# Performance work log

Hardware: AMD Instinct MI355X
Metric: run time of the kernel (lower is better)

The kernel has to match this reference:

```python
import jax, jax.numpy as jnp
import numpy as np

B, S, HE, HD = 32, 2048, 1024, 1024

def setup_inputs() -> dict:
    key = jax.random.key(0)
    k1, k2, k3, k4, k5 = jax.random.split(key, 5)
    enc_hiddens = jax.random.normal(k1, (B, S, HE), dtype=jnp.float32)
    dec_hidden = jax.random.normal(k2, (B, HD), dtype=jnp.float32)
    mask = jax.random.randint(k3, (B, S), 0, 2).astype(bool)  # True = masked out
    # params init uniform(-0.05, 0.05) as in init_weights
    W = jax.random.uniform(k4, (HD, HE + HD), dtype=jnp.float32, minval=-0.05, maxval=0.05)
    V = jax.random.uniform(k5, (1, HD), dtype=jnp.float32, minval=-0.05, maxval=0.05)
    return {"enc_hiddens": enc_hiddens, "dec_hidden": dec_hidden, "mask": mask, "W": W, "V": V}

def reference(enc_hiddens, dec_hidden, mask, W, V):
    # e = V^T tanh(W [enc; dec]) -- split W to avoid materializing the concat:
    # W @ [enc;dec] == W_enc @ enc + W_dec @ dec (same math, fused-friendly)
    HE_ = enc_hiddens.shape[-1]
    W_enc, W_dec = W[:, :HE_], W[:, HE_:]
    h = jnp.tanh(jnp.einsum('bse,de->bsd', enc_hiddens, W_enc)
                 + jnp.einsum('be,de->bd', dec_hidden, W_dec)[:, None, :])  # [B,S,HD]
    scores = jnp.einsum('bsd,od->bs', h, V)  # [B,S] (o==1 squeezed)
    scores = jnp.where(mask, -jnp.inf, scores)
    attn = jax.nn.softmax(scores, axis=1)[:, None, :]  # [B,1,S]
    ctx = jnp.einsum('bos,bse->be', attn, enc_hiddens)  # squeeze of bmm -> [B,HE]
    return (ctx, attn)
```

## Files before the change

### kernel.cpp

```cpp
#include <hip/hip_runtime.h>
#include <hip/hip_bf16.h>
#include <math.h>

#define BB 32
#define SS 2048
#define HE 1024
#define HD 1024
#define WROW (HE + HD)

typedef __attribute__((ext_vector_type(8))) short bf16x8;
typedef __attribute__((ext_vector_type(4))) float f32x4;
typedef __attribute__((ext_vector_type(16))) float f32x16;
typedef __attribute__((ext_vector_type(8))) unsigned short u16x8;

__device__ __forceinline__ unsigned short f2bf(float f) {
    union { float f; unsigned u; } v; v.f = f;
    unsigned r = v.u + 0x7fffu + ((v.u >> 16) & 1u);
    return (unsigned short)(r >> 16);
}

__device__ __forceinline__ unsigned int pk2(float x, float y) {
    union { __hip_bfloat162 h; unsigned int u; } c;
    c.h = __float22bfloat162_rn(float2{x, y});
    return c.u;
}

#define LGKM0()  asm volatile("s_waitcnt lgkmcnt(0)" ::: "memory")
#define BAR()    asm volatile("s_barrier" ::: "memory")

__global__ __launch_bounds__(256) void k_prep(const float* __restrict__ W,
                                              const float* __restrict__ dec,
                                              const int* __restrict__ mask,
                                              unsigned short* __restrict__ wf,
                                              float* __restrict__ proj,
                                              int* __restrict__ idx,
                                              int* __restrict__ cntblk) {
    __shared__ int cb[2048];
    __shared__ int cw[4], coff[5];
    const int bx = blockIdx.x, tid = threadIdx.x;
    if (bx < 32) {
        const int b = bx, w = tid >> 6, ln = tid & 63;
        const int base = w * 512;
        int cnt = 0;
        for (int r = 0; r < 8; r++) {
            int s = base + r * 64 + ln;
            int m = mask[b * SS + s];
            unsigned long long bal = __ballot(m == 0);
            int pos = __popcll(bal & ((1ull << ln) - 1ull));
            if (m == 0) cb[base + cnt + pos] = s;
            cnt += __popcll(bal);
        }
        if (ln == 0) cw[w] = cnt;
        __syncthreads();
        if (tid == 0) {
            coff[0] = 0;
            for (int q = 0; q < 4; q++) coff[q + 1] = coff[q] + cw[q];
        }
        __syncthreads();
        const int total = coff[4];
        for (int i = tid; i < total; i += 256) {
            int q = (i >= coff[1]) + (i >= coff[2]) + (i >= coff[3]);
            idx[b * SS + i] = cb[q * 512 + (i - coff[q])];
        }
        const int padded = (total + 63) & ~63;
        for (int i = total + tid; i < padded; i += 256) idx[b * SS + i] = (int)0x80000000;
        if (tid == 0) cntblk[b] = padded >> 6;
    } else if (bx < 544) {
        int i = (bx - 32) * 256 + tid;
        int d = i >> 7;
        int c = i & 127;
        const float4* src = (const float4*)(W + (size_t)d * WROW + c * 8);
        float4 a = src[0], b2 = src[1];
        u16x8 o;
        o[0] = f2bf(a.x);  o[1] = f2bf(a.y);  o[2] = f2bf(a.z);  o[3] = f2bf(a.w);
        o[4] = f2bf(b2.x); o[5] = f2bf(b2.y); o[6] = f2bf(b2.z); o[7] = f2bf(b2.w);
        int ks = c >> 1;
        int l  = (d & 31) + 32 * (c & 1);
        int g  = d >> 5;
        *(u16x8*)(wf + ((size_t)(g * 64 + ks) * 64 + l) * 8) = o;
    } else {
        const int dl = tid >> 6;
        const int b  = (tid >> 1) & 31;
        const int hf = tid & 1;
        const int d  = (bx - 544) * 4 + dl;
        const float* wrow = W + (size_t)d * WROW + HE + hf * 512;
        const float* dv   = dec + b * HD + hf * 512;
        float s = 0.f;
        #pragma unroll 4
        for (int e = 0; e < 512; e += 4) {
            float4 w4 = *(const float4*)(wrow + e);
            float4 x4 = *(const float4*)(dv + e);
            s += w4.x * x4.x + w4.y * x4.y + w4.z * x4.z + w4.w * x4.w;
        }
        s += __shfl_xor(s, 1, 64);
        if (hf == 0) proj[b * HD + d] = s;
    }
}

__global__ __launch_bounds__(512, 2) void k_scores_mfma8b(
        const float* __restrict__ enc,
        const unsigned short* __restrict__ wf,
        const float* __restrict__ V,
        const float* __restrict__ proj,
        const int* __restrict__ idx,
        const int* __restrict__ cntblk,
        float* __restrict__ psc,
        float* __restrict__ pZ,
        float* __restrict__ pnum) {
    __shared__ unsigned short SM[8192];

    const int lid = blockIdx.x;
    int b = -1, loc = 0;
    {
        int a = 0;
        #pragma unroll
        for (int i = 0; i < 32; i++) {
            int c = cntblk[i];
            if (lid >= a && lid < a + c) { b = i; loc = lid - a; }
            a += c;
        }
    }
    if (b < 0) return;
    const int lt0 = loc << 6;

    const int tid = threadIdx.x;
    const int wv = tid >> 6, ln = tid & 63, l31 = ln & 31, hi = ln >> 5;

    const int rid = idx[b * SS + lt0 + (tid >> 3)];
    const size_t arow = ((size_t)b * SS + (rid & 0xffff)) * 1024;

    f32x16 acc[2][4];
    #pragma unroll
    for (int m = 0; m < 2; m++)
        #pragma unroll
        for (int n = 0; n < 4; n++)
            #pragma unroll
            for (int r = 0; r < 16; r++) acc[m][n][r] = 0.f;

    float4 areg[2];
    bf16x8 bgE[8], bgF[8];

    #define LOAD_A(k) do { \
        const float4* g_ = (const float4*)(enc + arow + (k) + (tid & 7) * 8); \
        areg[0] = g_[0]; areg[1] = g_[1]; \
    } while (0)

    #define CVTW_A(buf) do { \
        int row_ = tid >> 3; \
        union { u16x8 s; uint4 u; } pk_; \
        pk_.u.x = pk2(areg[0].x, areg[0].y); \
        pk_.u.y = pk2(areg[0].z, areg[0].w); \
        pk_.u.z = pk2(areg[1].x, areg[1].y); \
        pk_.u.w = pk2(areg[1].z, areg[1].w); \
        *(u16x8*)&SM[(buf) * 4096 + row_ * 64 + (((tid & 7) ^ (row_ & 7)) << 3)] = pk_.s; \
    } while (0)

    #define LOADB(bgx, tt, ksb) do { \
        _Pragma("unroll") \
        for (int kk = 0; kk < 2; kk++) \
            _Pragma("unroll") \
            for (int n = 0; n < 4; n++) \
                bgx[kk * 4 + n] = *(const bf16x8*)(wf + ((size_t)((wv * 4 + n) * 64 + (tt) * 4 + (ksb) + kk) * 64 + ln) * 8); \
        } while (0)

    #define HALF(bg, ksb, Ac) do { \
        _Pragma("unroll") \
        for (int kk = 0; kk < 2; kk++) { \
            bf16x8 af0, af1; \
            { int c_ = ((ksb) + kk) * 2 + hi; int row_ = l31; \
              af0 = *(const bf16x8*)&(Ac)[row_ * 64 + ((c_ ^ (row_ & 7)) << 3)]; } \
            { int c_ = ((ksb) + kk) * 2 + hi; int row_ = 32 + l31; \
              af1 = *(const bf16x8*)&(Ac)[row_ * 64 + ((c_ ^ (row_ & 7)) << 3)]; } \
            __builtin_amdgcn_s_setprio(1); \
            _Pragma("unroll") \
            for (int n = 0; n < 4; n++) \
                acc[0][n] = __builtin_amdgcn_mfma_f32_32x32x16_bf16(af0, bg[kk * 4 + n], acc[0][n], 0, 0, 0); \
            _Pragma("unroll") \
            for (int n = 0; n < 4; n++) \
                acc[1][n] = __builtin_amdgcn_mfma_f32_32x32x16_bf16(af1, bg[kk * 4 + n], acc[1][n], 0, 0, 0); \
            __builtin_amdgcn_s_setprio(0); \
        } } while (0)

    LOADB(bgE, 0, 0); LOADB(bgF, 0, 2);
    LOAD_A(0);
    CVTW_A(0);
    LOAD_A(64);
    LGKM0(); BAR();

    for (int t = 0; t < 16; ++t) {
        const int cur = t & 1, nxt = cur ^ 1;
        const unsigned short* Ac = SM + cur * 4096;

        HALF(bgE, 0, Ac);

        if (t < 15) {
            LOADB(bgE, t + 1, 0);
            CVTW_A(nxt);
            if (t < 14) LOAD_A((t + 2) * 64);
        }

        HALF(bgF, 2, Ac);

        if (t < 15) {
            LOADB(bgF, t + 1, 2);
            LGKM0(); BAR();
        }
    }
    #undef LOAD_A
    #undef CVTW_A
    #undef LOADB
    #undef HALF

    float sc[2][16];
    #pragma unroll
    for (int m = 0; m < 2; m++)
        #pragma unroll
        for (int r = 0; r < 16; r++) sc[m][r] = 0.f;
    #pragma unroll
    for (int n = 0; n < 4; n++) {
        int d = wv * 128 + n * 32 + l31;
        float pd  = proj[b * 1024 + d];
        float vv  = V[d];
        float vv2 = 2.f * vv;
        #pragma unroll
        for (int m = 0; m < 2; m++)
            #pragma unroll
            for (int r = 0; r < 16; r++) {
                float y  = acc[m][n][r] + pd;
                float e2 = __expf(2.f * y);
                float rc = __builtin_amdgcn_rcpf(e2 + 1.f);
                sc[m][r] += vv - vv2 * rc;
            }
    }

    #pragma unroll
    for (int m = 0; m < 2; m++)
        #pragma unroll
        for (int r = 0; r < 16; r++) {
            float v = sc[m][r];
            v += __shfl_xor(v, 1, 64);
            v += __shfl_xor(v, 2, 64);
            v += __shfl_xor(v, 4, 64);
            v += __shfl_xor(v, 8, 64);
            v += __shfl_xor(v, 16, 64);
            sc[m][r] = v;
        }

    __syncthreads();
    float* redf = (float*)SM;
    float* pf   = (float*)SM + 512;
    int*   ri   = (int*)SM + 576;
    if (l31 == 0) {
        #pragma unroll
        for (int m = 0; m < 2; m++)
            #pragma unroll
            for (int r = 0; r < 16; r++) {
                int tok = m * 32 + (r & 3) + 8 * (r >> 2) + 4 * hi;
                redf[tok * 8 + wv] = sc[m][r];
            }
    }
    __syncthreads();
    if (tid < 64) {
        float s = 0.f;
        #pragma unroll
        for (int w = 0; w < 8; w++) s += redf[tid * 8 + w];
        int sidx = idx[b * SS + lt0 + tid];
        float p = (sidx >= 0) ? __expf(s) : 0.f;
        if (sidx >= 0) psc[b * SS + sidx] = p;
        pf[tid] = p;
        ri[tid] = sidx & 2047;
        float z = p;
        z += __shfl_xor(z, 1, 64);
        z += __shfl_xor(z, 2, 64);
        z += __shfl_xor(z, 4, 64);
        z += __shfl_xor(z, 8, 64);
        z += __shfl_xor(z, 16, 64);
        z += __shfl_xor(z, 32, 64);
        if (tid == 0) pZ[b * 32 + loc] = z;
    }
    __syncthreads();

    float n0 = 0.f, n1 = 0.f;
    const float* encb = enc + (size_t)b * SS * 1024;
    #pragma unroll 8
    for (int s2 = 0; s2 < 64; s2++) {
        float p = pf[s2];
        const float* rp = encb + (size_t)ri[s2] * 1024;
        n0 = fmaf(p, rp[tid], n0);
        n1 = fmaf(p, rp[tid + 512], n1);
    }
    float* pn = pnum + (size_t)(b * 32 + loc) * 1024;
    pn[tid]       = n0;
    pn[tid + 512] = n1;
}

__global__ __launch_bounds__(256) void k_finish(const float* __restrict__ pnum,
                                                const float* __restrict__ psc,
                                                const int* __restrict__ mask,
                                                const float* __restrict__ pZ,
                                                const int* __restrict__ cntblk,
                                                float* __restrict__ ctx,
                                                float* __restrict__ attn) {
    const int bx = blockIdx.x, tid = threadIdx.x;
    if (bx < 128) {
        int i = bx * 256 + tid;
        int b = i >> 10, e = i & 1023;
        const int c = cntblk[b];
        float Z = 0.f;
        for (int q = 0; q < c; q++) Z += pZ[b * 32 + q];
        float s = 0.f;
        for (int q = 0; q < c; q++) s += pnum[(size_t)(b * 32 + q) * 1024 + e];
        ctx[i] = s / Z;
    } else {
        const int b = bx - 128;
        const int c = cntblk[b];
        float Z = 0.f;
        for (int q = 0; q < c; q++) Z += pZ[b * 32 + q];
        float invZ = 1.f / Z;
        #pragma unroll
        for (int i = 0; i < 8; i++) {
            int s = tid + i * 256;
            int m = mask[b * SS + s];
            float p = m ? 0.f : psc[b * SS + s];
            attn[b * SS + s] = p * invZ;
        }
    }
}

__global__ __launch_bounds__(256) void k_projdec2(const float* __restrict__ dec,
                                                  const float* __restrict__ W,
                                                  float* __restrict__ proj) {
    const int tid = threadIdx.x;
    const int dl = tid >> 6;
    const int b  = (tid >> 1) & 31;
    const int hf = tid & 1;
    const int d  = blockIdx.x * 4 + dl;
    const float* wrow = W + (size_t)d * WROW + HE + hf * 512;
    const float* dv   = dec + b * HD + hf * 512;
    float s = 0.f;
    #pragma unroll 4
    for (int e = 0; e < 512; e += 4) {
        float4 w4 = *(const float4*)(wrow + e);
        float4 x4 = *(const float4*)(dv + e);
        s += w4.x * x4.x + w4.y * x4.y + w4.z * x4.z + w4.w * x4.w;
    }
    s += __shfl_xor(s, 1, 64);
    if (hf == 0) proj[b * HD + d] = s;
}

__global__ __launch_bounds__(256) void k_scores_f32(const float* __restrict__ enc,
                                                    const float* __restrict__ W,
                                                    const float* __restrict__ V,
                                                    const float* __restrict__ proj,
                                                    float* __restrict__ scores) {
    __shared__ float As[64][20];
    __shared__ float Bs[64][20];
    __shared__ float red[64][17];
    const int t0 = blockIdx.x * 64;
    const int b  = t0 >> 11;
    const int tid = threadIdx.x;
    const int tx = tid & 15, ty = tid >> 4;
    const int lrow = tid >> 2, lc4 = (tid & 3) * 4;
    float sc[4] = {0.f, 0.f, 0.f, 0.f};
    for (int n0 = 0; n0 < HD; n0 += 64) {
        float C[4][4] = {};
        for (int k0 = 0; k0 < HE; k0 += 16) {
            *(float4*)&As[lrow][lc4] = *(const float4*)(enc + (size_t)(t0 + lrow) * HE + k0 + lc4);
            *(float4*)&Bs[lrow][lc4] = *(const float4*)(W + (size_t)(n0 + lrow) * WROW + k0 + lc4);
            __syncthreads();
            #pragma unroll
            for (int k4 = 0; k4 < 16; k4 += 4) {
                float4 a[4], bb[4];
                #pragma unroll
                for (int i = 0; i < 4; i++) a[i]  = *(float4*)&As[ty * 4 + i][k4];
                #pragma unroll
                for (int j = 0; j < 4; j++) bb[j] = *(float4*)&Bs[tx * 4 + j][k4];
                #pragma unroll
                for (int i = 0; i < 4; i++)
                    #pragma unroll
                    for (int j = 0; j < 4; j++)
                        C[i][j] += a[i].x * bb[j].x + a[i].y * bb[j].y +
                                   a[i].z * bb[j].z + a[i].w * bb[j].w;
            }
            __syncthreads();
        }
        #pragma unroll
        for (int j = 0; j < 4; j++) {
            int d = n0 + tx * 4 + j;
            float pd = proj[b * HD + d];
            float v  = V[d];
            #pragma unroll
            for (int i = 0; i < 4; i++) {
                float y  = C[i][j] + pd;
                float e2 = __expf(2.f * y);
                sc[i] += v * (1.f - 2.f / (e2 + 1.f));
            }
        }
    }
    #pragma unroll
    for (int i = 0; i < 4; i++) red[ty * 4 + i][tx] = sc[i];
    __syncthreads();
    if (tid < 64) {
        float s = 0.f;
        #pragma unroll
        for (int x = 0; x < 16; x++) s += red[tid][x];
        scores[t0 + tid] = s;
    }
}

__global__ __launch_bounds__(256) void k_softmax_f32(float* __restrict__ sc_attn,
                                                     const int* __restrict__ mask) {
    __shared__ float sred[256];
    const int b = blockIdx.x, tid = threadIdx.x;
    float vals[8]; int msk[8];
    float lmax = -1e30f;
    #pragma unroll
    for (int i = 0; i < 8; i++) {
        int s = tid + i * 256;
        vals[i] = sc_attn[b * SS + s];
        msk[i]  = mask[b * SS + s];
        if (!msk[i]) lmax = fmaxf(lmax, vals[i]);
    }
    sred[tid] = lmax; __syncthreads();
    for (int off = 128; off > 0; off >>= 1) {
        if (tid < off) sred[tid] = fmaxf(sred[tid], sred[tid + off]);
        __syncthreads();
    }
    float m = sred[0];
    __syncthreads();
    float ex[8]; float lsum = 0.f;
    #pragma unroll
    for (int i = 0; i < 8; i++) { ex[i] = msk[i] ? 0.f : __expf(vals[i] - m); lsum += ex[i]; }
    sred[tid] = lsum; __syncthreads();
    for (int off = 128; off > 0; off >>= 1) {
        if (tid < off) sred[tid] += sred[tid + off];
        __syncthreads();
    }
    float inv = 1.f / sred[0];
    #pragma unroll
    for (int i = 0; i < 8; i++) sc_attn[b * SS + tid + i * 256] = ex[i] * inv;
}

__global__ __launch_bounds__(256) void k_ctx_atomic(const float* __restrict__ enc,
                                                    const float* __restrict__ attn,
                                                    float* __restrict__ ctx) {
    const int b = blockIdx.x;
    const int e = blockIdx.y * 256 + threadIdx.x;
    const int s0 = blockIdx.z * 256;
    float sum = 0.f;
    for (int s = s0; s < s0 + 256; s++)
        sum += attn[b * SS + s] * enc[((size_t)b * SS + s) * HE + e];
    atomicAdd(&ctx[b * HE + e], sum);
}

extern "C" void kernel_launch(void* const* d_in, const int* in_sizes, int n_in,
                              void* d_out, int out_size, void* d_ws, size_t ws_size,
                              hipStream_t stream) {
    const float* enc  = (const float*)d_in[0];
    const float* dec  = (const float*)d_in[1];
    const int*   mask = (const int*)d_in[2];
    const float* W    = (const float*)d_in[3];
    const float* V    = (const float*)d_in[4];

    float* out  = (float*)d_out;
    float* ctx  = out;
    float* attn = out + BB * HE;

    const size_t WF_OFF = 0, PROJ_OFF = 2097152, PSC_OFF = PROJ_OFF + 131072,
                 IDX_OFF = PSC_OFF + 262144, CNT_OFF = IDX_OFF + 262144,
                 PZ_OFF = CNT_OFF + 4096, PN_OFF = PZ_OFF + 4096,
                 WS_NEED = PN_OFF + 4194304;
    if (ws_size >= WS_NEED) {
        char* w = (char*)d_ws;
        unsigned short* wf = (unsigned short*)(w + WF_OFF);
        float* proj        = (float*)(w + PROJ_OFF);
        float* psc         = (float*)(w + PSC_OFF);
        int*   idx         = (int*)(w + IDX_OFF);
        int*   cntblk      = (int*)(w + CNT_OFF);
        float* pZ          = (float*)(w + PZ_OFF);
        float* pnum        = (float*)(w + PN_OFF);

        k_prep<<<800, 256, 0, stream>>>(W, dec, mask, wf, proj, idx, cntblk);
        k_scores_mfma8b<<<1024, 512, 0, stream>>>(enc, wf, V, proj, idx, cntblk,
                                                  psc, pZ, pnum);
        k_finish<<<160, 256, 0, stream>>>(pnum, psc, mask, pZ, cntblk, ctx, attn);
    } else {
        float* proj  = ctx;
        float* score = attn;
        k_projdec2<<<256, 256, 0, stream>>>(dec, W, proj);
        k_scores_f32<<<(BB * SS) / 64, 256, 0, stream>>>(enc, W, V, proj, score);
        k_softmax_f32<<<BB, 256, 0, stream>>>(score, mask);
        hipMemsetAsync(ctx, 0, (size_t)BB * HE * sizeof(float), stream);
        k_ctx_atomic<<<dim3(BB, HE / 256, 8), 256, 0, stream>>>(enc, attn, ctx);
    }
}
```

Measured before the change: 171.9 us.

## Split tail token tiles across blocks by HD slice to balance load

```diff
diff --git a/kernel.cpp b/kernel.cpp
--- a/kernel.cpp
+++ b/kernel.cpp
@@ -106,192 +106,347 @@
         const int* __restrict__ cntblk,
         float* __restrict__ psc,
         float* __restrict__ pZ,
-        float* __restrict__ pnum) {
-    __shared__ unsigned short SM[8192];
-
-    const int lid = blockIdx.x;
-    int b = -1, loc = 0;
-    {
-        int a = 0;
-        #pragma unroll
-        for (int i = 0; i < 32; i++) {
-            int c = cntblk[i];
-            if (lid >= a && lid < a + c) { b = i; loc = lid - a; }
-            a += c;
-        }
-    }
-    if (b < 0) return;
-    const int lt0 = loc << 6;
+        float* __restrict__ pnum,
+        float* __restrict__ scorebuf) {
+    __shared__ unsigned short SM[32768];
 
     const int tid = threadIdx.x;
     const int wv = tid >> 6, ln = tid & 63, l31 = ln & 31, hi = ln >> 5;
 
-    const int rid = idx[b * SS + lt0 + (tid >> 3)];
-    const size_t arow = ((size_t)b * SS + (rid & 0xffff)) * 1024;
-
-    f32x16 acc[2][4];
-    #pragma unroll
-    for (int m = 0; m < 2; m++)
-        #pragma unroll
-        for (int n = 0; n < 4; n++)
-            #pragma unroll
-            for (int r = 0; r < 16; r++) acc[m][n][r] = 0.f;
-
-    float4 areg[2];
-    bf16x8 bgE[8], bgF[8];
-
-    #define LOAD_A(k) do { \
-        const float4* g_ = (const float4*)(enc + arow + (k) + (tid & 7) * 8); \
-        areg[0] = g_[0]; areg[1] = g_[1]; \
-    } while (0)
-
-    #define CVTW_A(buf) do { \
-        int row_ = tid >> 3; \
-        union { u16x8 s; uint4 u; } pk_; \
-        pk_.u.x = pk2(areg[0].x, areg[0].y); \
-        pk_.u.y = pk2(areg[0].z, areg[0].w); \
-        pk_.u.z = pk2(areg[1].x, areg[1].y); \
-        pk_.u.w = pk2(areg[1].z, areg[1].w); \
-        *(u16x8*)&SM[(buf) * 4096 + row_ * 64 + (((tid & 7) ^ (row_ & 7)) << 3)] = pk_.s; \
-    } while (0)
-
-    #define LOADB(bgx, tt, ksb) do { \
-        _Pragma("unroll") \
-        for (int kk = 0; kk < 2; kk++) \
-            _Pragma("unroll") \
-            for (int n = 0; n < 4; n++) \
-                bgx[kk * 4 + n] = *(const bf16x8*)(wf + ((size_t)((wv * 4 + n) * 64 + (tt) * 4 + (ksb) + kk) * 64 + ln) * 8); \
-        } while (0)
-
-    #define HALF(bg, ksb, Ac) do { \
-        _Pragma("unroll") \
-        for (int kk = 0; kk < 2; kk++) { \
-            bf16x8 af0, af1; \
-            { int c_ = ((ksb) + kk) * 2 + hi; int row_ = l31; \
-              af0 = *(const bf16x8*)&(Ac)[row_ * 64 + ((c_ ^ (row_ & 7)) << 3)]; } \
-            { int c_ = ((ksb) + kk) * 2 + hi; int row_ = 32 + l31; \
-              af1 = *(const bf16x8*)&(Ac)[row_ * 64 + ((c_ ^ (row_ & 7)) << 3)]; } \
-            __builtin_amdgcn_s_setprio(1); \
-            _Pragma("unroll") \
-            for (int n = 0; n < 4; n++) \
-                acc[0][n] = __builtin_amdgcn_mfma_f32_32x32x16_bf16(af0, bg[kk * 4 + n], acc[0][n], 0, 0, 0); \
-            _Pragma("unroll") \
-            for (int n = 0; n < 4; n++) \
-                acc[1][n] = __builtin_amdgcn_mfma_f32_32x32x16_bf16(af1, bg[kk * 4 + n], acc[1][n], 0, 0, 0); \
-            __builtin_amdgcn_s_setprio(0); \
-        } } while (0)
-
-    LOADB(bgE, 0, 0); LOADB(bgF, 0, 2);
-    LOAD_A(0);
-    CVTW_A(0);
-    LOAD_A(64);
-    LGKM0(); BAR();
-
-    for (int t = 0; t < 16; ++t) {
-        const int cur = t & 1, nxt = cur ^ 1;
-        const unsigned short* Ac = SM + cur * 4096;
-
-        HALF(bgE, 0, Ac);
-
-        if (t < 15) {
-            LOADB(bgE, t + 1, 0);
-            CVTW_A(nxt);
-            if (t < 14) LOAD_A((t + 2) * 64);
-        }
-
-        HALF(bgF, 2, Ac);
-
-        if (t < 15) {
-            LOADB(bgF, t + 1, 2);
-            LGKM0(); BAR();
-        }
-    }
-    #undef LOAD_A
-    #undef CVTW_A
-    #undef LOADB
-    #undef HALF
-
-    float sc[2][16];
-    #pragma unroll
-    for (int m = 0; m < 2; m++)
-        #pragma unroll
-        for (int r = 0; r < 16; r++) sc[m][r] = 0.f;
-    #pragma unroll
-    for (int n = 0; n < 4; n++) {
-        int d = wv * 128 + n * 32 + l31;
-        float pd  = proj[b * 1024 + d];
-        float vv  = V[d];
-        float vv2 = 2.f * vv;
+    if (blockIdx.x < 512) {
+        const int lid = blockIdx.x;
+        int b = -1, loc = 0;
+        {
+            int a = 0;
+            #pragma unroll
+            for (int i = 0; i < 32; i++) {
+                int c = cntblk[i];
+                if (lid >= a && lid < a + c) { b = i; loc = lid - a; }
+                a += c;
+            }
+        }
+        if (b < 0) return;
+        const int lt0 = loc << 6;
+
+        const int rid = idx[b * SS + lt0 + (tid >> 3)];
+        const size_t arow = ((size_t)b * SS + (rid & 0xffff)) * 1024;
+
+        f32x16 acc[2][4];
         #pragma unroll
         for (int m = 0; m < 2; m++)
             #pragma unroll
-            for (int r = 0; r < 16; r++) {
-                float y  = acc[m][n][r] + pd;
-                float e2 = __expf(2.f * y);
-                float rc = __builtin_amdgcn_rcpf(e2 + 1.f);
-                sc[m][r] += vv - vv2 * rc;
-            }
-    }
-
-    #pragma unroll
-    for (int m = 0; m < 2; m++)
-        #pragma unroll
-        for (int r = 0; r < 16; r++) {
-            float v = sc[m][r];
-            v += __shfl_xor(v, 1, 64);
-            v += __shfl_xor(v, 2, 64);
-            v += __shfl_xor(v, 4, 64);
-            v += __shfl_xor(v, 8, 64);
-            v += __shfl_xor(v, 16, 64);
-            sc[m][r] = v;
-        }
-
-    __syncthreads();
-    float* redf = (float*)SM;
-    float* pf   = (float*)SM + 512;
-    int*   ri   = (int*)SM + 576;
-    if (l31 == 0) {
+            for (int n = 0; n < 4; n++)
+                #pragma unroll
+                for (int r = 0; r < 16; r++) acc[m][n][r] = 0.f;
+
+        float4 areg[2];
+        bf16x8 bgE[8], bgF[8];
+
+        #define LOAD_A(k) do { \
+            const float4* g_ = (const float4*)(enc + arow + (k) + (tid & 7) * 8); \
+            areg[0] = g_[0]; areg[1] = g_[1]; \
+        } while (0)
+
+        #define CVTW_A(buf) do { \
+            int row_ = tid >> 3; \
+            union { u16x8 s; uint4 u; } pk_; \
+            pk_.u.x = pk2(areg[0].x, areg[0].y); \
+            pk_.u.y = pk2(areg[0].z, areg[0].w); \
+            pk_.u.z = pk2(areg[1].x, areg[1].y); \
+            pk_.u.w = pk2(areg[1].z, areg[1].w); \
+            *(u16x8*)&SM[(buf) * 4096 + row_ * 64 + (((tid & 7) ^ (row_ & 7)) << 3)] = pk_.s; \
+        } while (0)
+
+        #define LOADB(bgx, tt, ksb) do { \
+            _Pragma("unroll") \
+            for (int kk = 0; kk < 2; kk++) \
+                _Pragma("unroll") \
+                for (int n = 0; n < 4; n++) \
+                    bgx[kk * 4 + n] = *(const bf16x8*)(wf + ((size_t)((wv * 4 + n) * 64 + (tt) * 4 + (ksb) + kk) * 64 + ln) * 8); \
+            } while (0)
+
+        #define HALF(bg, ksb, Ac) do { \
+            _Pragma("unroll") \
+            for (int kk = 0; kk < 2; kk++) { \
+                bf16x8 af0, af1; \
+                { int c_ = ((ksb) + kk) * 2 + hi; int row_ = l31; \
+                  af0 = *(const bf16x8*)&(Ac)[row_ * 64 + ((c_ ^ (row_ & 7)) << 3)]; } \
+                { int c_ = ((ksb) + kk) * 2 + hi; int row_ = 32 + l31; \
+                  af1 = *(const bf16x8*)&(Ac)[row_ * 64 + ((c_ ^ (row_ & 7)) << 3)]; } \
+                __builtin_amdgcn_s_setprio(1); \
+                _Pragma("unroll") \
+                for (int n = 0; n < 4; n++) \
+                    acc[0][n] = __builtin_amdgcn_mfma_f32_32x32x16_bf16(af0, bg[kk * 4 + n], acc[0][n], 0, 0, 0); \
+                _Pragma("unroll") \
+                for (int n = 0; n < 4; n++) \
+                    acc[1][n] = __builtin_amdgcn_mfma_f32_32x32x16_bf16(af1, bg[kk * 4 + n], acc[1][n], 0, 0, 0); \
+                __builtin_amdgcn_s_setprio(0); \
+            } } while (0)
+
+        LOADB(bgE, 0, 0); LOADB(bgF, 0, 2);
+        LOAD_A(0);
+        CVTW_A(0);
+        LOAD_A(64);
+        LGKM0(); BAR();
+
+        for (int t = 0; t < 16; ++t) {
+            const int cur = t & 1, nxt = cur ^ 1;
+            const unsigned short* Ac = SM + cur * 4096;
+
+            HALF(bgE, 0, Ac);
+            if (t < 15) {
+                LOADB(bgE, t + 1, 0);
+                CVTW_A(nxt);
+                if (t < 14) LOAD_A((t + 2) * 64);
+            }
+            HALF(bgF, 2, Ac);
+            if (t < 15) {
+                LOADB(bgF, t + 1, 2);
+                LGKM0(); BAR();
+            }
+        }
+        #undef LOAD_A
+        #undef CVTW_A
+        #undef LOADB
+        #undef HALF
+
+        float sc[2][16];
         #pragma unroll
         for (int m = 0; m < 2; m++)
             #pragma unroll
+            for (int r = 0; r < 16; r++) sc[m][r] = 0.f;
+        #pragma unroll
+        for (int n = 0; n < 4; n++) {
+            int d = wv * 128 + n * 32 + l31;
+            float pd  = proj[b * 1024 + d];
+            float vv  = V[d];
+            float vv2 = 2.f * vv;
+            #pragma unroll
+            for (int m = 0; m < 2; m++)
+                #pragma unroll
+                for (int r = 0; r < 16; r++) {
+                    float y  = acc[m][n][r] + pd;
+                    float e2 = __expf(2.f * y);
+                    float rc = __builtin_amdgcn_rcpf(e2 + 1.f);
+                    sc[m][r] += vv - vv2 * rc;
+                }
+        }
+        #pragma unroll
+        for (int m = 0; m < 2; m++)
+            #pragma unroll
             for (int r = 0; r < 16; r++) {
-                int tok = m * 32 + (r & 3) + 8 * (r >> 2) + 4 * hi;
-                redf[tok * 8 + wv] = sc[m][r];
-            }
-    }
-    __syncthreads();
-    if (tid < 64) {
-        float s = 0.f;
-        #pragma unroll
-        for (int w = 0; w < 8; w++) s += redf[tid * 8 + w];
-        int sidx = idx[b * SS + lt0 + tid];
-        float p = (sidx >= 0) ? __expf(s) : 0.f;
-        if (sidx >= 0) psc[b * SS + sidx] = p;
-        pf[tid] = p;
-        ri[tid] = sidx & 2047;
-        float z = p;
-        z += __shfl_xor(z, 1, 64);
-        z += __shfl_xor(z, 2, 64);
-        z += __shfl_xor(z, 4, 64);
-        z += __shfl_xor(z, 8, 64);
-        z += __shfl_xor(z, 16, 64);
-        z += __shfl_xor(z, 32, 64);
-        if (tid == 0) pZ[b * 32 + loc] = z;
-    }
-    __syncthreads();
-
-    float n0 = 0.f, n1 = 0.f;
-    const float* encb = enc + (size_t)b * SS * 1024;
-    #pragma unroll 8
-    for (int s2 = 0; s2 < 64; s2++) {
-        float p = pf[s2];
-        const float* rp = encb + (size_t)ri[s2] * 1024;
-        n0 = fmaf(p, rp[tid], n0);
-        n1 = fmaf(p, rp[tid + 512], n1);
-    }
-    float* pn = pnum + (size_t)(b * 32 + loc) * 1024;
-    pn[tid]       = n0;
-    pn[tid + 512] = n1;
+                float v = sc[m][r];
+                v += __shfl_xor(v, 1, 64);
+                v += __shfl_xor(v, 2, 64);
+                v += __shfl_xor(v, 4, 64);
+                v += __shfl_xor(v, 8, 64);
+                v += __shfl_xor(v, 16, 64);
+                sc[m][r] = v;
+            }
+
+        __syncthreads();
+        float* redf = (float*)SM;
+        float* pf   = (float*)SM + 512;
+        int*   ri   = (int*)SM + 576;
+        if (l31 == 0) {
+            #pragma unroll
+            for (int m = 0; m < 2; m++)
+                #pragma unroll
+                for (int r = 0; r < 16; r++) {
+                    int tok = m * 32 + (r & 3) + 8 * (r >> 2) + 4 * hi;
+                    redf[tok * 8 + wv] = sc[m][r];
+                }
+        }
+        __syncthreads();
+        if (tid < 64) {
+            float s = 0.f;
+            #pragma unroll
+            for (int w = 0; w < 8; w++) s += redf[tid * 8 + w];
+            int sidx = idx[b * SS + lt0 + tid];
+            float p = (sidx >= 0) ? __expf(s) : 0.f;
+            if (sidx >= 0) psc[b * SS + sidx] = p;
+            pf[tid] = p;
+            ri[tid] = sidx & 2047;
+            float z = p;
+            z += __shfl_xor(z, 1, 64);
+            z += __shfl_xor(z, 2, 64);
+            z += __shfl_xor(z, 4, 64);
+            z += __shfl_xor(z, 8, 64);
+            z += __shfl_xor(z, 16, 64);
+            z += __shfl_xor(z, 32, 64);
+            if (tid == 0) pZ[b * 32 + loc] = z;
+        }
+        __syncthreads();
+
+        float n0 = 0.f, n1 = 0.f;
+        const float* encb = enc + (size_t)b * SS * 1024;
+        #pragma unroll 8
+        for (int s2 = 0; s2 < 64; s2++) {
+            float p = pf[s2];
+            const float* rp = encb + (size_t)ri[s2] * 1024;
+            n0 = fmaf(p, rp[tid], n0);
+            n1 = fmaf(p, rp[tid + 512], n1);
+        }
+        float* pn = pnum + (size_t)(b * 32 + loc) * 1024;
+        pn[tid]       = n0;
+        pn[tid + 512] = n1;
+    } else {
+        const int e = blockIdx.x - 512;
+        const int dblk = e & 7;
+        for (int ex = e >> 3; ex < 512; ex += 64) {
+            const int lid = 512 + ex;
+            int b = -1, loc = 0;
+            {
+                int a = 0;
+                #pragma unroll
+                for (int i = 0; i < 32; i++) {
+                    int c = cntblk[i];
+                    if (lid >= a && lid < a + c) { b = i; loc = lid - a; }
+                    a += c;
+                }
+            }
+            if (b < 0) break;
+            const int lt0 = loc << 6;
+
+            f32x16 tacc[2][4];
+            #pragma unroll
+            for (int m = 0; m < 2; m++)
+                #pragma unroll
+                for (int n = 0; n < 4; n++)
+                    #pragma unroll
+                    for (int r = 0; r < 16; r++) tacc[m][n][r] = 0.f;
+
+            unsigned short* slab = SM + 4096 * wv;
+            #pragma unroll
+            for (int q = 0; q < 2; q++) {
+                const int tt = 2 * wv + q;
+                #pragma unroll
+                for (int it = 0; it < 8; it++) {
+                    int row = it * 8 + (ln >> 3);
+                    int kc  = ln & 7;
+                    int r2  = idx[b * SS + lt0 + row];
+                    const float4* g_ = (const float4*)(enc +
+                        ((size_t)b * SS + (r2 & 0xffff)) * 1024 + tt * 64 + kc * 8);
+                    float4 a0 = g_[0], a1 = g_[1];
+                    union { u16x8 s; uint4 u; } pk_;
+                    pk_.u.x = pk2(a0.x, a0.y); pk_.u.y = pk2(a0.z, a0.w);
+                    pk_.u.z = pk2(a1.x, a1.y); pk_.u.w = pk2(a1.z, a1.w);
+                    *(u16x8*)&slab[row * 64 + ((kc ^ (row & 7)) << 3)] = pk_.s;
+                }
+                LGKM0();
+                #pragma unroll
+                for (int ks = 0; ks < 4; ks++) {
+                    bf16x8 bg[4];
+                    #pragma unroll
+                    for (int n = 0; n < 4; n++)
+                        bg[n] = *(const bf16x8*)(wf +
+                            ((size_t)((dblk * 4 + n) * 64 + tt * 4 + ks) * 64 + ln) * 8);
+                    int c0 = ks * 2 + hi;
+                    bf16x8 af0 = *(const bf16x8*)&slab[l31 * 64 + ((c0 ^ (l31 & 7)) << 3)];
+                    bf16x8 af1 = *(const bf16x8*)&slab[(32 + l31) * 64 + ((c0 ^ ((32 + l31) & 7)) << 3)];
+                    #pragma unroll
+                    for (int n = 0; n < 4; n++)
+                        tacc[0][n] = __builtin_amdgcn_mfma_f32_32x32x16_bf16(af0, bg[n], tacc[0][n], 0, 0, 0);
+                    #pragma unroll
+                    for (int n = 0; n < 4; n++)
+                        tacc[1][n] = __builtin_amdgcn_mfma_f32_32x32x16_bf16(af1, bg[n], tacc[1][n], 0, 0, 0);
+                }
+            }
+            BAR();
+            float* rt = (float*)SM;
+            for (int i = tid; i < 8192; i += 512) rt[i] = 0.f;
+            BAR();
+            #pragma unroll
+            for (int m = 0; m < 2; m++)
+                #pragma unroll
+                for (int n = 0; n < 4; n++)
+                    #pragma unroll
+                    for (int r = 0; r < 16; r++) {
+                        int row = m * 32 + (r & 3) + 8 * (r >> 2) + 4 * hi;
+                        int col = n * 32 + l31;
+                        atomicAdd(&rt[row * 128 + col], tacc[m][n][r]);
+                    }
+            BAR();
+            {
+                int tok = tid >> 3, dq = tid & 7;
+                float s = 0.f;
+                #pragma unroll
+                for (int j = 0; j < 16; j++) {
+                    int dl = dq * 16 + j;
+                    int d  = dblk * 128 + dl;
+                    float y  = rt[tok * 128 + dl] + proj[b * 1024 + d];
+                    float e2 = __expf(2.f * y);
+                    float rc = __builtin_amdgcn_rcpf(e2 + 1.f);
+                    s += V[d] * (1.f - 2.f * rc);
+                }
+                s += __shfl_xor(s, 1, 64);
+                s += __shfl_xor(s, 2, 64);
+                s += __shfl_xor(s, 4, 64);
+                if (dq == 0) {
+                    int sidx = idx[b * SS + lt0 + tok];
+                    if (sidx >= 0) atomicAdd(&scorebuf[b * SS + sidx], s);
+                }
+            }
+            BAR();
+        }
+    }
+}
+
+__global__ __launch_bounds__(256) void k_fixup(const float* __restrict__ scorebuf,
+                                               const float* __restrict__ enc,
+                                               const int* __restrict__ idx,
+                                               const int* __restrict__ cntblk,
+                                               float* __restrict__ psc,
+                                               float* __restrict__ pZ,
+                                               float* __restrict__ pnum) {
+    __shared__ float pf[64];
+    __shared__ int   ri[64];
+    const int tid = threadIdx.x;
+    for (int ex = blockIdx.x; ex < 512; ex += 64) {
+        const int lid = 512 + ex;
+        int b = -1, loc = 0;
+        {
+            int a = 0;
+            #pragma unroll
+            for (int i = 0; i < 32; i++) {
+                int c = cntblk[i];
+                if (lid >= a && lid < a + c) { b = i; loc = lid - a; }
+                a += c;
+            }
+        }
+        if (b < 0) break;
+        const int lt0 = loc << 6;
+        if (tid < 64) {
+            int sidx = idx[b * SS + lt0 + tid];
+            float p = 0.f;
+            if (sidx >= 0) {
+                p = __expf(scorebuf[b * SS + sidx]);
+                psc[b * SS + sidx] = p;
+            }
+            pf[tid] = p;
+            ri[tid] = sidx & 2047;
+            float z = p;
+            z += __shfl_xor(z, 1, 64);
+            z += __shfl_xor(z, 2, 64);
+            z += __shfl_xor(z, 4, 64);
+            z += __shfl_xor(z, 8, 64);
+            z += __shfl_xor(z, 16, 64);
+            z += __shfl_xor(z, 32, 64);
+            if (tid == 0) pZ[b * 32 + loc] = z;
+        }
+        __syncthreads();
+        float4 acc = {0.f, 0.f, 0.f, 0.f};
+        const float4* e4 = (const float4*)(enc + (size_t)b * SS * 1024);
+        #pragma unroll 4
+        for (int s = 0; s < 64; s++) {
+            float p = pf[s];
+            float4 v = e4[(size_t)ri[s] * 256 + tid];
+            acc.x = fmaf(p, v.x, acc.x); acc.y = fmaf(p, v.y, acc.y);
+            acc.z = fmaf(p, v.z, acc.z); acc.w = fmaf(p, v.w, acc.w);
+        }
+        *(float4*)(pnum + (size_t)(b * 32 + loc) * 1024 + tid * 4) = acc;
+        __syncthreads();
+    }
 }
 
 __global__ __launch_bounds__(256) void k_finish(const float* __restrict__ pnum,
@@ -469,7 +624,7 @@
     const size_t WF_OFF = 0, PROJ_OFF = 2097152, PSC_OFF = PROJ_OFF + 131072,
                  IDX_OFF = PSC_OFF + 262144, CNT_OFF = IDX_OFF + 262144,
                  PZ_OFF = CNT_OFF + 4096, PN_OFF = PZ_OFF + 4096,
-                 WS_NEED = PN_OFF + 4194304;
+                 SB_OFF = PN_OFF + 4194304, WS_NEED = SB_OFF + 262144;
     if (ws_size >= WS_NEED) {
         char* w = (char*)d_ws;
         unsigned short* wf = (unsigned short*)(w + WF_OFF);
@@ -479,10 +634,13 @@
         int*   cntblk      = (int*)(w + CNT_OFF);
         float* pZ          = (float*)(w + PZ_OFF);
         float* pnum        = (float*)(w + PN_OFF);
-
+        float* scorebuf    = (float*)(w + SB_OFF);
+
+        hipMemsetAsync(scorebuf, 0, 262144, stream);
         k_prep<<<800, 256, 0, stream>>>(W, dec, mask, wf, proj, idx, cntblk);
         k_scores_mfma8b<<<1024, 512, 0, stream>>>(enc, wf, V, proj, idx, cntblk,
-                                                  psc, pZ, pnum);
+                                                  psc, pZ, pnum, scorebuf);
+        k_fixup<<<64, 256, 0, stream>>>(scorebuf, enc, idx, cntblk, psc, pZ, pnum);
         k_finish<<<160, 256, 0, stream>>>(pnum, psc, mask, pZ, cntblk, ctx, attn);
     } else {
         float* proj  = ctx;
```

Result: slower. 242.9 us (+41.3%).

## Pack unmasked tokens across batches into dense 64-row tiles

Applied to the files above, without the earlier changes.

```diff
diff --git a/kernel.cpp b/kernel.cpp
--- a/kernel.cpp
+++ b/kernel.cpp
@@ -34,23 +34,25 @@
                                               unsigned short* __restrict__ wf,
                                               float* __restrict__ proj,
                                               int* __restrict__ idx,
-                                              int* __restrict__ cntblk) {
+                                              int* __restrict__ cnt,
+                                              float* __restrict__ Zg) {
     __shared__ int cb[2048];
     __shared__ int cw[4], coff[5];
     const int bx = blockIdx.x, tid = threadIdx.x;
     if (bx < 32) {
         const int b = bx, w = tid >> 6, ln = tid & 63;
         const int base = w * 512;
-        int cnt = 0;
+        if (b == 0 && tid < 32) Zg[tid] = 0.f;
+        int cntw = 0;
         for (int r = 0; r < 8; r++) {
             int s = base + r * 64 + ln;
             int m = mask[b * SS + s];
             unsigned long long bal = __ballot(m == 0);
             int pos = __popcll(bal & ((1ull << ln) - 1ull));
-            if (m == 0) cb[base + cnt + pos] = s;
-            cnt += __popcll(bal);
-        }
-        if (ln == 0) cw[w] = cnt;
+            if (m == 0) cb[base + cntw + pos] = s;
+            cntw += __popcll(bal);
+        }
+        if (ln == 0) cw[w] = cntw;
         __syncthreads();
         if (tid == 0) {
             coff[0] = 0;
@@ -62,9 +64,7 @@
             int q = (i >= coff[1]) + (i >= coff[2]) + (i >= coff[3]);
             idx[b * SS + i] = cb[q * 512 + (i - coff[q])];
         }
-        const int padded = (total + 63) & ~63;
-        for (int i = total + tid; i < padded; i += 256) idx[b * SS + i] = (int)0x80000000;
-        if (tid == 0) cntblk[b] = padded >> 6;
+        if (tid == 0) cnt[b] = total;
     } else if (bx < 544) {
         int i = (bx - 32) * 256 + tid;
         int d = i >> 7;
@@ -103,31 +103,31 @@
         const float* __restrict__ V,
         const float* __restrict__ proj,
         const int* __restrict__ idx,
-        const int* __restrict__ cntblk,
+        const int* __restrict__ cnt,
         float* __restrict__ psc,
-        float* __restrict__ pZ,
+        float* __restrict__ Zg,
         float* __restrict__ pnum) {
     __shared__ unsigned short SM[8192];
 
-    const int lid = blockIdx.x;
-    int b = -1, loc = 0;
-    {
-        int a = 0;
-        #pragma unroll
-        for (int i = 0; i < 32; i++) {
-            int c = cntblk[i];
-            if (lid >= a && lid < a + c) { b = i; loc = lid - a; }
-            a += c;
-        }
-    }
-    if (b < 0) return;
-    const int lt0 = loc << 6;
-
+    const int g = blockIdx.x;
     const int tid = threadIdx.x;
     const int wv = tid >> 6, ln = tid & 63, l31 = ln & 31, hi = ln >> 5;
 
-    const int rid = idx[b * SS + lt0 + (tid >> 3)];
-    const size_t arow = ((size_t)b * SS + (rid & 0xffff)) * 1024;
+    size_t arow;
+    {
+        const int P = g * 64 + (tid >> 3);
+        int total = 0, bj = -1, offj = 0;
+        #pragma unroll
+        for (int i = 0; i < 32; i++) {
+            int c = cnt[i];
+            if (P >= total && P < total + c) { bj = i; offj = total; }
+            total += c;
+        }
+        if (g * 64 >= total) return;
+        size_t rowid = 0;
+        if (bj >= 0) rowid = (size_t)bj * SS + idx[bj * SS + (P - offj)];
+        arow = rowid * 1024;
+    }
 
     f32x16 acc[2][4];
     #pragma unroll
@@ -211,6 +211,40 @@
     #undef LOADB
     #undef HALF
 
+    __syncthreads();
+    float* redf = (float*)SM;
+    float* pf   = (float*)SM + 512;
+    int*   ri   = (int*)SM + 576;
+    int*   meta = (int*)SM + 640;
+    int*   lv   = (int*)SM + 644;
+    if (tid < 64) {
+        const int P = g * 64 + tid;
+        int total = 0, b2 = -1, off2 = 0;
+        #pragma unroll
+        for (int i = 0; i < 32; i++) {
+            int c = cnt[i];
+            if (P >= total && P < total + c) { b2 = i; off2 = total; }
+            total += c;
+        }
+        int live = (b2 >= 0);
+        int row2 = live ? (b2 * SS + idx[b2 * SS + (P - off2)]) : 0;
+        ri[tid] = row2;
+        lv[tid] = live;
+        int blo = __shfl(b2, 0, 64);
+        int bhr = __shfl(b2, 63, 64);
+        int bhi = (bhr < 0) ? blo : bhr;
+        unsigned long long bm = __ballot(live && b2 == bhi && bhi != blo);
+        if (tid == 0) {
+            meta[0] = blo; meta[1] = bhi;
+            meta[2] = (int)(unsigned)(bm & 0xffffffffull);
+            meta[3] = (int)(unsigned)(bm >> 32);
+        }
+    }
+    __syncthreads();
+    const int blo = meta[0], bhi = meta[1];
+    const unsigned long long bm =
+        ((unsigned long long)(unsigned)meta[3] << 32) | (unsigned)meta[2];
+
     float sc[2][16];
     #pragma unroll
     for (int m = 0; m < 2; m++)
@@ -219,13 +253,16 @@
     #pragma unroll
     for (int n = 0; n < 4; n++) {
         int d = wv * 128 + n * 32 + l31;
-        float pd  = proj[b * 1024 + d];
+        float pdl = proj[blo * 1024 + d];
+        float pdh = proj[bhi * 1024 + d];
         float vv  = V[d];
         float vv2 = 2.f * vv;
         #pragma unroll
         for (int m = 0; m < 2; m++)
             #pragma unroll
             for (int r = 0; r < 16; r++) {
+                int tok = m * 32 + (r & 3) + 8 * (r >> 2) + 4 * hi;
+                float pd = ((bm >> tok) & 1ull) ? pdh : pdl;
                 float y  = acc[m][n][r] + pd;
                 float e2 = __expf(2.f * y);
                 float rc = __builtin_amdgcn_rcpf(e2 + 1.f);
@@ -246,10 +283,6 @@
             sc[m][r] = v;
         }
 
-    __syncthreads();
-    float* redf = (float*)SM;
-    float* pf   = (float*)SM + 512;
-    int*   ri   = (int*)SM + 576;
     if (l31 == 0) {
         #pragma unroll
         for (int m = 0; m < 2; m++)
@@ -264,59 +297,69 @@
         float s = 0.f;
         #pragma unroll
         for (int w = 0; w < 8; w++) s += redf[tid * 8 + w];
-        int sidx = idx[b * SS + lt0 + tid];
-        float p = (sidx >= 0) ? __expf(s) : 0.f;
-        if (sidx >= 0) psc[b * SS + sidx] = p;
+        int live = lv[tid];
+        float p = live ? __expf(s) : 0.f;
+        if (live) psc[ri[tid]] = p;
         pf[tid] = p;
-        ri[tid] = sidx & 2047;
-        float z = p;
-        z += __shfl_xor(z, 1, 64);
-        z += __shfl_xor(z, 2, 64);
-        z += __shfl_xor(z, 4, 64);
-        z += __shfl_xor(z, 8, 64);
-        z += __shfl_xor(z, 16, 64);
-        z += __shfl_xor(z, 32, 64);
-        if (tid == 0) pZ[b * 32 + loc] = z;
+        int selh = (int)((bm >> tid) & 1ull);
+        float zh = selh ? p : 0.f;
+        float zl = p - zh;
+        #pragma unroll
+        for (int o = 1; o < 64; o <<= 1) {
+            zl += __shfl_xor(zl, o, 64);
+            zh += __shfl_xor(zh, o, 64);
+        }
+        if (tid == 0) {
+            atomicAdd(&Zg[blo], zl);
+            if (bhi != blo) atomicAdd(&Zg[bhi], zh);
+        }
     }
     __syncthreads();
 
-    float n0 = 0.f, n1 = 0.f;
-    const float* encb = enc + (size_t)b * SS * 1024;
+    float n0l = 0.f, n1l = 0.f, n0h = 0.f, n1h = 0.f;
     #pragma unroll 8
     for (int s2 = 0; s2 < 64; s2++) {
-        float p = pf[s2];
-        const float* rp = encb + (size_t)ri[s2] * 1024;
-        n0 = fmaf(p, rp[tid], n0);
-        n1 = fmaf(p, rp[tid + 512], n1);
-    }
-    float* pn = pnum + (size_t)(b * 32 + loc) * 1024;
-    pn[tid]       = n0;
-    pn[tid + 512] = n1;
+        float p  = pf[s2];
+        float ph = ((bm >> s2) & 1ull) ? p : 0.f;
+        float pl = p - ph;
+        const float* rp = enc + (size_t)ri[s2] * 1024;
+        float v0 = rp[tid], v1 = rp[tid + 512];
+        n0l = fmaf(pl, v0, n0l);
+        n1l = fmaf(pl, v1, n1l);
+        n0h = fmaf(ph, v0, n0h);
+        n1h = fmaf(ph, v1, n1h);
+    }
+    float* pn = pnum + (size_t)g * 2048;
+    pn[tid]        = n0l;
+    pn[tid + 512]  = n1l;
+    pn[tid + 1024] = n0h;
+    pn[tid + 1536] = n1h;
 }
 
 __global__ __launch_bounds__(256) void k_finish(const float* __restrict__ pnum,
                                                 const float* __restrict__ psc,
                                                 const int* __restrict__ mask,
-                                                const float* __restrict__ pZ,
-                                                const int* __restrict__ cntblk,
+                                                const float* __restrict__ Zg,
+                                                const int* __restrict__ cnt,
                                                 float* __restrict__ ctx,
                                                 float* __restrict__ attn) {
     const int bx = blockIdx.x, tid = threadIdx.x;
     if (bx < 128) {
         int i = bx * 256 + tid;
         int b = i >> 10, e = i & 1023;
-        const int c = cntblk[b];
-        float Z = 0.f;
-        for (int q = 0; q < c; q++) Z += pZ[b * 32 + q];
+        int off = 0;
+        for (int q = 0; q < b; q++) off += cnt[q];
+        const int cb = cnt[b];
+        const int c0 = off >> 6, c1 = (off + cb - 1) >> 6;
         float s = 0.f;
-        for (int q = 0; q < c; q++) s += pnum[(size_t)(b * 32 + q) * 1024 + e];
-        ctx[i] = s / Z;
+        for (int c = c0; c <= c1; c++) {
+            int slot = (c == c0 && (off & 63)) ? 1 : 0;
+            s += pnum[(size_t)c * 2048 + slot * 1024 + e];
+        }
+        ctx[i] = s / Zg[b];
     } else {
         const int b = bx - 128;
-        const int c = cntblk[b];
-        float Z = 0.f;
-        for (int q = 0; q < c; q++) Z += pZ[b * 32 + q];
-        float invZ = 1.f / Z;
+        float invZ = 1.f / Zg[b];
         #pragma unroll
         for (int i = 0; i < 8; i++) {
             int s = tid + i * 256;
@@ -468,22 +511,22 @@
 
     const size_t WF_OFF = 0, PROJ_OFF = 2097152, PSC_OFF = PROJ_OFF + 131072,
                  IDX_OFF = PSC_OFF + 262144, CNT_OFF = IDX_OFF + 262144,
-                 PZ_OFF = CNT_OFF + 4096, PN_OFF = PZ_OFF + 4096,
-                 WS_NEED = PN_OFF + 4194304;
+                 ZG_OFF = CNT_OFF + 4096, PN_OFF = ZG_OFF + 4096,
+                 WS_NEED = PN_OFF + (size_t)576 * 2048 * 4;
     if (ws_size >= WS_NEED) {
         char* w = (char*)d_ws;
         unsigned short* wf = (unsigned short*)(w + WF_OFF);
         float* proj        = (float*)(w + PROJ_OFF);
         float* psc         = (float*)(w + PSC_OFF);
         int*   idx         = (int*)(w + IDX_OFF);
-        int*   cntblk      = (int*)(w + CNT_OFF);
-        float* pZ          = (float*)(w + PZ_OFF);
+        int*   cnt         = (int*)(w + CNT_OFF);
+        float* Zg          = (float*)(w + ZG_OFF);
         float* pnum        = (float*)(w + PN_OFF);
 
-        k_prep<<<800, 256, 0, stream>>>(W, dec, mask, wf, proj, idx, cntblk);
-        k_scores_mfma8b<<<1024, 512, 0, stream>>>(enc, wf, V, proj, idx, cntblk,
-                                                  psc, pZ, pnum);
-        k_finish<<<160, 256, 0, stream>>>(pnum, psc, mask, pZ, cntblk, ctx, attn);
+        k_prep<<<800, 256, 0, stream>>>(W, dec, mask, wf, proj, idx, cnt, Zg);
+        k_scores_mfma8b<<<576, 512, 0, stream>>>(enc, wf, V, proj, idx, cnt,
+                                                 psc, Zg, pnum);
+        k_finish<<<160, 256, 0, stream>>>(pnum, psc, mask, Zg, cnt, ctx, attn);
     } else {
         float* proj  = ctx;
         float* score = attn;
```

New measurement: 176.2 us. +2.5%, slower.
